# Performance work log

Measured on AMD Instinct MI355X. Metric: run time of the kernel, lower is better.

Reference implementation:

```python
import jax, jax.numpy as jnp
import numpy as np

MIN_NORM = 1e-15
EPS = 4e-3  # fp32 boundary epsilon used by HGCN PoincareBall


def _norm(x):
    return jnp.maximum(jnp.linalg.norm(x, axis=-1, keepdims=True), MIN_NORM)


def _artanh(x):
    return jnp.arctanh(jnp.clip(x, -1.0 + 1e-7, 1.0 - 1e-7))


def proj(x, c):
    # clip points to the open Poincare ball of curvature c
    norm = _norm(x)
    maxnorm = (1.0 - EPS) / jnp.sqrt(c)
    return jnp.where(norm > maxnorm, x / norm * maxnorm, x)


def expmap0(u, c):
    sc = jnp.sqrt(c)
    un = _norm(u)
    return jnp.tanh(sc * un) * u / (sc * un)


def logmap0(p, c):
    sc = jnp.sqrt(c)
    pn = _norm(p)
    return _artanh(sc * pn) * p / (pn * sc)


def mobius_add(x, y, c):
    x2 = jnp.sum(x * x, axis=-1, keepdims=True)
    y2 = jnp.sum(y * y, axis=-1, keepdims=True)
    xy = jnp.sum(x * y, axis=-1, keepdims=True)
    num = (1.0 + 2.0 * c * xy + c * y2) * x + (1.0 - c * x2) * y
    den = 1.0 + 2.0 * c * xy + (c ** 2) * x2 * y2
    return num / jnp.maximum(den, MIN_NORM)


def _mobius_from_mx(mx, x, c):
    # shared tail of mobius_matvec: mx is the Euclidean product, x the input points
    sc = jnp.sqrt(c)
    x_norm = _norm(x)            # [..., 1]
    mx_norm = _norm(mx)          # [..., 1]
    res = jnp.tanh(mx_norm / x_norm * _artanh(sc * x_norm)) * mx / (mx_norm * sc)
    zero_row = jnp.all(mx == 0, axis=-1, keepdims=True)
    return jnp.where(zero_row, jnp.zeros_like(res), res)


def mobius_matvec(m, x, c):
    # standard form: mx = x @ m^T   (m: [out, in], x: [N, in])
    return _mobius_from_mx(x @ m.T, x, c)


def hyp_linear(x, W, b, c):
    hw = proj(expmap0(W, c), c)             # proj_tan0 is identity on PoincareBall
    res = proj(mobius_matvec(hw, x, c), c)
    hb = proj(expmap0(b[None, :], c), c)
    return proj(mobius_add(res, hb, c), c)


def hyp_agg(h, adj, W, b, c):
    hw = proj(expmap0(W, c), c)
    support = mobius_matvec(hw, h, c)       # [N, O]
    # mobius_matvec(support, adj, c): Euclidean part is adj @ support,
    # hyperbolic rescale uses row norms of adj (the 'x' argument)
    out = _mobius_from_mx(adj @ support, adj, c)
    out = mobius_add(out, b[None, :], c)    # raw Euclidean bias, as in source
    return proj(out, c)


def hyp_act(h, c):
    xt = jax.nn.leaky_relu(logmap0(h, c))   # default slope 0.01 == F.leaky_relu
    return proj(expmap0(xt, c), 1.0 - c)    # NOTE: source projects with 1-c


def setup_inputs() -> dict:
    key = jax.random.key(0)
    kx, ka, kw1, kw2, kb2 = jax.random.split(key, 5)
    N, IN, OUT = 8192, 512, 128
    x = jax.random.normal(kx, (N, IN), dtype=jnp.float32) * 0.1
    adj = jax.random.uniform(ka, (N, N), dtype=jnp.float32) * (1.0 / N)
    c = jnp.full((1,), 0.7, dtype=jnp.float32)
    glorot = np.sqrt(6.0 / (IN + OUT))
    lin_weight = jax.random.uniform(kw1, (OUT, IN), minval=-glorot, maxval=glorot, dtype=jnp.float32)
    lin_bias = jnp.zeros((OUT,), dtype=jnp.float32)
    stdv = 1.0 / np.sqrt(OUT)
    agg_weight = jax.random.uniform(kw2, (OUT, OUT), minval=-stdv, maxval=stdv, dtype=jnp.float32)
    agg_bias = jax.random.uniform(kb2, (OUT,), minval=-stdv, maxval=stdv, dtype=jnp.float32)
    return {"x": x, "adj": adj, "c": c, "lin_weight": lin_weight, "lin_bias": lin_bias,
            "agg_weight": agg_weight, "agg_bias": agg_bias}


def reference(x, adj, c, lin_weight, lin_bias, agg_weight, agg_bias):
    h = hyp_linear(x, lin_weight, lin_bias, c)
    h = hyp_agg(h, adj, agg_weight, agg_bias, c)
    return hyp_act(h, c)
```

## Files before the change

### kernel.cpp

```cpp
#include <hip/hip_runtime.h>
#include <math.h>


#define MINN 1e-15f

typedef __bf16 bf16x8 __attribute__((ext_vector_type(8)));
typedef float  f32x4  __attribute__((ext_vector_type(4)));

__device__ __forceinline__ unsigned short f2bf(float f) {
  unsigned int u = __float_as_uint(f);
  u += 0x7FFFu + ((u >> 16) & 1u);
  return (unsigned short)(u >> 16);
}

__device__ __forceinline__ float artanh_clip(float z) {
  const float B = (float)(1.0 - 1e-7);
  z = fminf(fmaxf(z, -B), B);
  return 0.5f * logf((1.0f + z) / (1.0f - z));
}

__device__ __forceinline__ float red16(float v) {
  v += __shfl_xor(v, 1, 16);
  v += __shfl_xor(v, 2, 16);
  v += __shfl_xor(v, 4, 16);
  v += __shfl_xor(v, 8, 16);
  return v;
}
__device__ __forceinline__ int red16_and(int v) {
  v &= __shfl_xor(v, 1, 16);
  v &= __shfl_xor(v, 2, 16);
  v &= __shfl_xor(v, 4, 16);
  v &= __shfl_xor(v, 8, 16);
  return v;
}

__device__ __forceinline__ float block_reduce_128(float v, float* red, int t) {
  #pragma unroll
  for (int m = 1; m < 64; m <<= 1) v += __shfl_xor(v, m, 64);
  if ((t & 63) == 0) red[t >> 6] = v;
  __syncthreads();
  return red[0] + red[1];
}

__device__ __forceinline__ size_t bswz(int k, int n) {
  return ((size_t)(((k >> 5) * 8 + (n >> 4)) * 64 + ((k >> 3) & 3) * 16 +
                   (n & 15))) * 8 + (k & 7);
}

__global__ __launch_bounds__(128) void prep_kernel(
    const float* __restrict__ lw, const float* __restrict__ aw,
    const float* __restrict__ lb, const float* __restrict__ cp,
    unsigned short* __restrict__ B1, unsigned short* __restrict__ B2,
    float* __restrict__ hb)
{
  const float c  = cp[0];
  const float sc = sqrtf(c);
  const float maxn = 0.996f / sc;
  const int b = blockIdx.x, t = threadIdx.x;
  __shared__ float red[2];

  if (b < 128) {
    const int o = b;
    float4 v = ((const float4*)(lw + (size_t)o * 512))[t];
    float ss = block_reduce_128(v.x*v.x + v.y*v.y + v.z*v.z + v.w*v.w, red, t);
    float un = fmaxf(sqrtf(ss), MINN);
    float f  = tanhf(sc * un) / (sc * un);
    float nn = f * un;
    if (nn > maxn) f *= maxn / nn;
    float vals[4] = {v.x, v.y, v.z, v.w};
    #pragma unroll
    for (int i = 0; i < 4; ++i)
      B1[bswz(4 * t + i, o)] = f2bf(f * vals[i]);
  } else if (b < 256) {
    const int n = b - 128;
    float v = aw[(size_t)n * 128 + t];
    float ss = block_reduce_128(v * v, red, t);
    float un = fmaxf(sqrtf(ss), MINN);
    float f  = tanhf(sc * un) / (sc * un);
    float nn = f * un;
    if (nn > maxn) f *= maxn / nn;
    B2[bswz(t, n)] = f2bf(f * v);
  } else {
    float v = lb[t];
    float ss = block_reduce_128(v * v, red, t);
    float un = fmaxf(sqrtf(ss), MINN);
    float f  = tanhf(sc * un) / (sc * un);
    float nn = f * un;
    if (nn > maxn) f *= maxn / nn;
    hb[t] = f * v;
  }
}

template <int MODE>
__global__ __launch_bounds__(256) void hyp_gemm(
    const float* __restrict__ A, const bf16x8* __restrict__ Bf, int K,
    const float* __restrict__ cp, const float* __restrict__ yvec,
    void* __restrict__ outp)
{
  __shared__ unsigned short a_lds[2][16][72];
  __shared__ float mx_lds[16][132];
  const int t    = threadIdx.x;
  const int row0 = blockIdx.x * 16;
  const int lane = t & 63, w = t >> 6;
  const int quad = lane >> 4, l15 = lane & 15;
  const int srow = t >> 4, skg = t & 15;
  const float c  = cp[0];
  const float sc = sqrtf(c);
  const float maxn = 0.996f / sc;
  const int nsteps = K >> 6;

  f32x4 acc0 = {0.f, 0.f, 0.f, 0.f};
  f32x4 acc1 = {0.f, 0.f, 0.f, 0.f};
  float asum = 0.f;
  const float* Ap = A + (size_t)(row0 + srow) * K + skg * 4;

  {
    float4 aR = *(const float4*)Ap;
    asum += aR.x*aR.x + aR.y*aR.y + aR.z*aR.z + aR.w*aR.w;
    union { unsigned short u[4]; uint2 v2; } pk;
    pk.u[0] = f2bf(aR.x); pk.u[1] = f2bf(aR.y);
    pk.u[2] = f2bf(aR.z); pk.u[3] = f2bf(aR.w);
    *(uint2*)&a_lds[0][srow][skg * 4] = pk.v2;
  }
  __syncthreads();

  int cur = 0;
  for (int s = 0; s < nsteps; ++s) {
    const size_t fb = (size_t)(16 * s) * 64 + lane;
    bf16x8 b00 = Bf[fb + (2 * w + 0) * 64];
    bf16x8 b01 = Bf[fb + (2 * w + 1) * 64];
    bf16x8 b10 = Bf[fb + (8 + 2 * w + 0) * 64];
    bf16x8 b11 = Bf[fb + (8 + 2 * w + 1) * 64];

    const bool more = (s + 1 < nsteps);
    float4 aN;
    if (more) aN = *(const float4*)(Ap + (size_t)(s + 1) * 64);

    bf16x8 a0 = *(const bf16x8*)&a_lds[cur][l15][quad * 8];
    bf16x8 a1 = *(const bf16x8*)&a_lds[cur][l15][32 + quad * 8];
    acc0 = __builtin_amdgcn_mfma_f32_16x16x32_bf16(a0, b00, acc0, 0, 0, 0);
    acc1 = __builtin_amdgcn_mfma_f32_16x16x32_bf16(a0, b01, acc1, 0, 0, 0);
    acc0 = __builtin_amdgcn_mfma_f32_16x16x32_bf16(a1, b10, acc0, 0, 0, 0);
    acc1 = __builtin_amdgcn_mfma_f32_16x16x32_bf16(a1, b11, acc1, 0, 0, 0);

    if (more) {
      asum += aN.x*aN.x + aN.y*aN.y + aN.z*aN.z + aN.w*aN.w;
      union { unsigned short u[4]; uint2 v2; } pk;
      pk.u[0] = f2bf(aN.x); pk.u[1] = f2bf(aN.y);
      pk.u[2] = f2bf(aN.z); pk.u[3] = f2bf(aN.w);
      *(uint2*)&a_lds[cur ^ 1][srow][skg * 4] = pk.v2;
      cur ^= 1;
    }
    __syncthreads();
  }

  #pragma unroll
  for (int r = 0; r < 4; ++r) {
    mx_lds[quad * 4 + r][32 * w + l15]      = acc0[r];
    mx_lds[quad * 4 + r][32 * w + 16 + l15] = acc1[r];
  }
  __syncthreads();

  const int row = t >> 4, j0 = t & 15;
  float v[8];
  {
    float4 q0 = *(const float4*)&mx_lds[row][j0 * 8];
    float4 q1 = *(const float4*)&mx_lds[row][j0 * 8 + 4];
    v[0]=q0.x; v[1]=q0.y; v[2]=q0.z; v[3]=q0.w;
    v[4]=q1.x; v[5]=q1.y; v[6]=q1.z; v[7]=q1.w;
  }
  float mxss_l = 0.f; int zf = 1;
  #pragma unroll
  for (int i = 0; i < 8; ++i) { mxss_l += v[i] * v[i]; zf &= (v[i] == 0.f); }
  const float mxss = red16(mxss_l);
  const float xss  = red16(asum);
  zf = red16_and(zf);

  const float xn  = fmaxf(sqrtf(xss), MINN);
  const float mxn = fmaxf(sqrtf(mxss), MINN);
  float f1 = 0.f;
  if (!zf) f1 = tanhf(mxn / xn * artanh_clip(sc * xn)) / (mxn * sc);

  if (MODE == 2) {
    const int k = row0 + row;
    unsigned short* Bo = (unsigned short*)outp;
    const size_t base = ((size_t)(((k >> 5) * 8 + (j0 >> 1)) * 64 +
                         ((k >> 3) & 3) * 16 + 8 * (j0 & 1))) * 8 + (k & 7);
    #pragma unroll
    for (int i = 0; i < 8; ++i)
      Bo[base + (size_t)i * 8] = f2bf(f1 * v[i]);
    return;
  }

  float yv[8];
  {
    float4 q0 = ((const float4*)yvec)[j0 * 2];
    float4 q1 = ((const float4*)yvec)[j0 * 2 + 1];
    yv[0]=q0.x; yv[1]=q0.y; yv[2]=q0.z; yv[3]=q0.w;
    yv[4]=q1.x; yv[5]=q1.y; yv[6]=q1.z; yv[7]=q1.w;
  }

  float g = f1;
  if (MODE == 1) {
    float rn = f1 * mxn;
    if (rn > maxn) g = f1 * (maxn / rn);
  }

  float xy_l = 0.f, y2_l = 0.f;
  float o8[8];
  #pragma unroll
  for (int i = 0; i < 8; ++i) {
    o8[i] = g * v[i];
    xy_l += o8[i] * yv[i];
    y2_l += yv[i] * yv[i];
  }
  const float xy = red16(xy_l), y2 = red16(y2_l);
  const float x2 = g * g * mxss;
  const float den = fmaxf(1.0f + 2.0f * c * xy + c * c * x2 * y2, MINN);
  const float ca = (1.0f + 2.0f * c * xy + c * y2) / den;
  const float cb = (1.0f - c * x2) / den;
  float h8[8]; float hss_l = 0.f;
  #pragma unroll
  for (int i = 0; i < 8; ++i) {
    h8[i] = ca * o8[i] + cb * yv[i];
    hss_l += h8[i] * h8[i];
  }
  const float hss = red16(hss_l);
  const float hn  = fmaxf(sqrtf(hss), MINN);
  const float s2  = (hn > maxn) ? maxn / hn : 1.0f;

  float* orow = (float*)outp + (size_t)(row0 + row) * 128 + j0 * 8;

  if (MODE == 1) {
    float4 o0 = make_float4(s2*h8[0], s2*h8[1], s2*h8[2], s2*h8[3]);
    float4 o1 = make_float4(s2*h8[4], s2*h8[5], s2*h8[6], s2*h8[7]);
    *(float4*)orow = o0; *(float4*)(orow + 4) = o1;
    return;
  }

  const float pn = fmaxf(s2 * hn, MINN);
  const float lf = artanh_clip(sc * pn) / (pn * sc);
  float xt[8]; float uss_l = 0.f;
  #pragma unroll
  for (int i = 0; i < 8; ++i) {
    float l = lf * (s2 * h8[i]);
    xt[i] = (l >= 0.f) ? l : 0.01f * l;
    uss_l += xt[i] * xt[i];
  }
  const float uss = red16(uss_l);
  const float un  = fmaxf(sqrtf(uss), MINN);
  const float ef  = tanhf(sc * un) / (sc * un);
  const float on  = ef * un;
  const float maxn2 = 0.996f / sqrtf(1.0f - c);
  const float s3 = (on > maxn2) ? maxn2 / on : 1.0f;
  float4 o0 = make_float4(s3*ef*xt[0], s3*ef*xt[1], s3*ef*xt[2], s3*ef*xt[3]);
  float4 o1 = make_float4(s3*ef*xt[4], s3*ef*xt[5], s3*ef*xt[6], s3*ef*xt[7]);
  *(float4*)orow = o0; *(float4*)(orow + 4) = o1;
}

extern "C" void kernel_launch(void* const* d_in, const int* in_sizes, int n_in,
                              void* d_out, int out_size, void* d_ws, size_t ws_size,
                              hipStream_t stream)
{
  const float* x   = (const float*)d_in[0];
  const float* adj = (const float*)d_in[1];
  const float* cp  = (const float*)d_in[2];
  const float* lw  = (const float*)d_in[3];
  const float* lb  = (const float*)d_in[4];
  const float* aw  = (const float*)d_in[5];
  const float* ab  = (const float*)d_in[6];
  float* out = (float*)d_out;

  char* ws = (char*)d_ws;
  unsigned short* B1sw = (unsigned short*)(ws);
  unsigned short* B2sw = (unsigned short*)(ws + 131072);
  unsigned short* B3sw = (unsigned short*)(ws + 163840);
  float*          hb   = (float*)(ws + 2260992);
  float*          h    = (float*)(ws + 2261504);

  prep_kernel<<<257, 128, 0, stream>>>(lw, aw, lb, cp, B1sw, B2sw, hb);
  hyp_gemm<1><<<512, 256, 0, stream>>>(x,   (const bf16x8*)B1sw, 512,  cp, hb, h);
  hyp_gemm<2><<<512, 256, 0, stream>>>(h,   (const bf16x8*)B2sw, 128,  cp, nullptr, B3sw);
  hyp_gemm<3><<<512, 256, 0, stream>>>(adj, (const bf16x8*)B3sw, 8192, cp, ab, out);
}
```

Baseline: 447.5 us.

## Split K across waves in hyp_gemm, loading A directly into registers

```diff
diff --git a/kernel.cpp b/kernel.cpp
--- a/kernel.cpp
+++ b/kernel.cpp
@@ -92,88 +92,88 @@
 }
 
 template <int MODE>
-__global__ __launch_bounds__(256) void hyp_gemm(
+__global__ __launch_bounds__(256, 2) void hyp_gemm(
     const float* __restrict__ A, const bf16x8* __restrict__ Bf, int K,
     const float* __restrict__ cp, const float* __restrict__ yvec,
     void* __restrict__ outp)
 {
-  __shared__ unsigned short a_lds[2][16][72];
-  __shared__ float mx_lds[16][132];
+  __shared__ float part[4][16][132];
+  __shared__ float asw[4][16];
   const int t    = threadIdx.x;
+  const int w    = t >> 6, lane = t & 63;
+  const int quad = lane >> 4, l15 = lane & 15;
   const int row0 = blockIdx.x * 16;
-  const int lane = t & 63, w = t >> 6;
-  const int quad = lane >> 4, l15 = lane & 15;
-  const int srow = t >> 4, skg = t & 15;
   const float c  = cp[0];
   const float sc = sqrtf(c);
   const float maxn = 0.996f / sc;
-  const int nsteps = K >> 6;
-
-  f32x4 acc0 = {0.f, 0.f, 0.f, 0.f};
-  f32x4 acc1 = {0.f, 0.f, 0.f, 0.f};
+
+  const int Kw     = K >> 2;
+  const int nsteps = Kw >> 5;
+  const int k0w    = w * Kw;
+
+  f32x4 acc[8] = {};
   float asum = 0.f;
-  const float* Ap = A + (size_t)(row0 + srow) * K + skg * 4;
-
-  {
-    float4 aR = *(const float4*)Ap;
-    asum += aR.x*aR.x + aR.y*aR.y + aR.z*aR.z + aR.w*aR.w;
-    union { unsigned short u[4]; uint2 v2; } pk;
-    pk.u[0] = f2bf(aR.x); pk.u[1] = f2bf(aR.y);
-    pk.u[2] = f2bf(aR.z); pk.u[3] = f2bf(aR.w);
-    *(uint2*)&a_lds[0][srow][skg * 4] = pk.v2;
-  }
-  __syncthreads();
-
-  int cur = 0;
+
+  const float*  Ap = A + (size_t)(row0 + l15) * K + k0w + quad * 8;
+  const bf16x8* Bp = Bf + (size_t)(k0w >> 5) * 512 + lane;
+
+  float4 a0 = *(const float4*)(Ap);
+  float4 a1 = *(const float4*)(Ap + 4);
+  bf16x8 b[8];
+  #pragma unroll
+  for (int i = 0; i < 8; ++i) b[i] = Bp[i * 64];
+
   for (int s = 0; s < nsteps; ++s) {
-    const size_t fb = (size_t)(16 * s) * 64 + lane;
-    bf16x8 b00 = Bf[fb + (2 * w + 0) * 64];
-    bf16x8 b01 = Bf[fb + (2 * w + 1) * 64];
-    bf16x8 b10 = Bf[fb + (8 + 2 * w + 0) * 64];
-    bf16x8 b11 = Bf[fb + (8 + 2 * w + 1) * 64];
-
+    float4 na0, na1; bf16x8 nb[8];
     const bool more = (s + 1 < nsteps);
-    float4 aN;
-    if (more) aN = *(const float4*)(Ap + (size_t)(s + 1) * 64);
-
-    bf16x8 a0 = *(const bf16x8*)&a_lds[cur][l15][quad * 8];
-    bf16x8 a1 = *(const bf16x8*)&a_lds[cur][l15][32 + quad * 8];
-    acc0 = __builtin_amdgcn_mfma_f32_16x16x32_bf16(a0, b00, acc0, 0, 0, 0);
-    acc1 = __builtin_amdgcn_mfma_f32_16x16x32_bf16(a0, b01, acc1, 0, 0, 0);
-    acc0 = __builtin_amdgcn_mfma_f32_16x16x32_bf16(a1, b10, acc0, 0, 0, 0);
-    acc1 = __builtin_amdgcn_mfma_f32_16x16x32_bf16(a1, b11, acc1, 0, 0, 0);
-
     if (more) {
-      asum += aN.x*aN.x + aN.y*aN.y + aN.z*aN.z + aN.w*aN.w;
-      union { unsigned short u[4]; uint2 v2; } pk;
-      pk.u[0] = f2bf(aN.x); pk.u[1] = f2bf(aN.y);
-      pk.u[2] = f2bf(aN.z); pk.u[3] = f2bf(aN.w);
-      *(uint2*)&a_lds[cur ^ 1][srow][skg * 4] = pk.v2;
-      cur ^= 1;
+      const float* Ap2 = Ap + (size_t)(s + 1) * 32;
+      na0 = *(const float4*)(Ap2);
+      na1 = *(const float4*)(Ap2 + 4);
+      const bf16x8* Bp2 = Bp + (size_t)(s + 1) * 512;
+      #pragma unroll
+      for (int i = 0; i < 8; ++i) nb[i] = Bp2[i * 64];
     }
-    __syncthreads();
-  }
-
-  #pragma unroll
-  for (int r = 0; r < 4; ++r) {
-    mx_lds[quad * 4 + r][32 * w + l15]      = acc0[r];
-    mx_lds[quad * 4 + r][32 * w + 16 + l15] = acc1[r];
-  }
+    asum += a0.x*a0.x + a0.y*a0.y + a0.z*a0.z + a0.w*a0.w
+          + a1.x*a1.x + a1.y*a1.y + a1.z*a1.z + a1.w*a1.w;
+    union { unsigned short u[8]; bf16x8 v; } pk;
+    pk.u[0] = f2bf(a0.x); pk.u[1] = f2bf(a0.y);
+    pk.u[2] = f2bf(a0.z); pk.u[3] = f2bf(a0.w);
+    pk.u[4] = f2bf(a1.x); pk.u[5] = f2bf(a1.y);
+    pk.u[6] = f2bf(a1.z); pk.u[7] = f2bf(a1.w);
+    #pragma unroll
+    for (int i = 0; i < 8; ++i)
+      acc[i] = __builtin_amdgcn_mfma_f32_16x16x32_bf16(pk.v, b[i], acc[i],
+                                                       0, 0, 0);
+    if (more) {
+      a0 = na0; a1 = na1;
+      #pragma unroll
+      for (int i = 0; i < 8; ++i) b[i] = nb[i];
+    }
+  }
+
+  asum += __shfl_xor(asum, 16, 64);
+  asum += __shfl_xor(asum, 32, 64);
+  #pragma unroll
+  for (int i = 0; i < 8; ++i)
+    #pragma unroll
+    for (int r = 0; r < 4; ++r)
+      part[w][quad * 4 + r][i * 16 + l15] = acc[i][r];
+  if (lane < 16) asw[w][l15] = asum;
   __syncthreads();
 
   const int row = t >> 4, j0 = t & 15;
   float v[8];
-  {
-    float4 q0 = *(const float4*)&mx_lds[row][j0 * 8];
-    float4 q1 = *(const float4*)&mx_lds[row][j0 * 8 + 4];
-    v[0]=q0.x; v[1]=q0.y; v[2]=q0.z; v[3]=q0.w;
-    v[4]=q1.x; v[5]=q1.y; v[6]=q1.z; v[7]=q1.w;
-  }
+  #pragma unroll
+  for (int i = 0; i < 8; ++i)
+    v[i] = part[0][row][j0 * 8 + i] + part[1][row][j0 * 8 + i]
+         + part[2][row][j0 * 8 + i] + part[3][row][j0 * 8 + i];
+  const float xss = asw[0][row] + asw[1][row] + asw[2][row] + asw[3][row];
+
   float mxss_l = 0.f; int zf = 1;
   #pragma unroll
   for (int i = 0; i < 8; ++i) { mxss_l += v[i] * v[i]; zf &= (v[i] == 0.f); }
   const float mxss = red16(mxss_l);
-  const float xss  = red16(asum);
   zf = red16_and(zf);
 
   const float xn  = fmaxf(sqrtf(xss), MINN);
```

Result: faster. 438.0 us (-2.1%).
